# Optimization experiments

Measured on AMD Instinct MI355X. Metric: run time of the kernel, lower is better.

## Reference

```python
import jax, jax.numpy as jnp
import numpy as np

T, H, E = 1024, 2048, 32
I = 1024            # moe_intermediate_size
K = 8               # num_experts_per_token
G = 4               # num_expert_group
TOPK_GROUP = 2
N_SHARED = 2
IS = I * N_SHARED   # shared-expert intermediate
RSF = 2.5           # routed_scaling_factor


def setup_inputs() -> dict:
    key = jax.random.key(0)
    ks = jax.random.split(key, 9)
    s = 0.02
    return {
        "hidden_states": jax.random.normal(ks[0], (T, H), jnp.float32),
        "gate_w": jax.random.normal(ks[1], (H, E), jnp.float32) * s,
        "corr_bias": jax.random.normal(ks[2], (E,), jnp.float32) * s,
        "w_gate": jax.random.normal(ks[3], (E, H, I), jnp.float32) * s,
        "w_up": jax.random.normal(ks[4], (E, H, I), jnp.float32) * s,
        "w_down": jax.random.normal(ks[5], (E, I, H), jnp.float32) * s,
        "sw_gate": jax.random.normal(ks[6], (H, IS), jnp.float32) * s,
        "sw_up": jax.random.normal(ks[7], (H, IS), jnp.float32) * s,
        "sw_down": jax.random.normal(ks[8], (IS, H), jnp.float32) * s,
    }


def _route(x, gate_w, corr_bias):
    # biased grouped top-k (DeepSeek-V3 style sigmoid routing)
    logits = x @ gate_w                      # [T,E]
    scores = jax.nn.sigmoid(logits)
    sfc = scores + corr_bias[None, :]        # scores for choice
    grp = sfc.reshape(-1, G, E // G)
    # group score = sum of top-2 biased scores within the group
    grp_score = jax.lax.top_k(grp, 2)[0].sum(-1)          # [T,G]
    _, gidx = jax.lax.top_k(grp_score, TOPK_GROUP)        # [T,topk_group]
    rows = jnp.arange(sfc.shape[0])[:, None]
    gmask = jnp.zeros((sfc.shape[0], G), sfc.dtype).at[rows, gidx].set(1.0)
    emask = jnp.repeat(gmask, E // G, axis=1)             # [T,E]
    masked = jnp.where(emask > 0, sfc, -jnp.inf)
    _, idx = jax.lax.top_k(masked, K)                     # [T,K]
    w = jnp.take_along_axis(scores, idx, axis=1)          # unbiased scores
    w = w / w.sum(-1, keepdims=True)                      # renormalize
    w = w * RSF                                           # routed scaling
    combine = jnp.zeros((sfc.shape[0], E), x.dtype).at[rows, idx].add(w)
    return combine                                        # dense [T,E] combine weights


def reference(hidden_states, gate_w, corr_bias, w_gate, w_up, w_down,
              sw_gate, sw_up, sw_down):
    x = hidden_states
    # shared experts (SiLU-gated MLP)
    shared = (jax.nn.silu(x @ sw_gate) * (x @ sw_up)) @ sw_down   # [T,H]
    # routing
    combine = _route(x, gate_w, corr_bias)                        # [T,E]
    # routed experts (dense grouped-GEMM reference)
    g = jnp.einsum('th,ehi->tei', x, w_gate)
    u = jnp.einsum('th,ehi->tei', x, w_up)
    a = jax.nn.silu(g) * u                                        # [T,E,I]
    y = jnp.einsum('tei,eih->teh', a, w_down)                     # [T,E,H]
    routed = jnp.einsum('teh,te->th', y, combine)
    return routed + shared
```

## Files before the change

kernel.cpp:

```cpp
#include <hip/hip_runtime.h>

#define T_TOK 1024
#define H_DIM 2048
#define E_NUM 32
#define I_DIM 1024
#define IS_DIM 2048

typedef float  f32x4 __attribute__((ext_vector_type(4)));
typedef short  s16x8 __attribute__((ext_vector_type(8)));
typedef unsigned short u16x4 __attribute__((ext_vector_type(4)));
typedef unsigned short u16x8 __attribute__((ext_vector_type(8)));

__device__ __forceinline__ unsigned short f2bf(float f) {
    unsigned u = __builtin_bit_cast(unsigned, f);
    u = (u + 0x7fffu + ((u >> 16) & 1u)) >> 16;
    return (unsigned short)u;
}
__device__ __forceinline__ float bf2f(unsigned short h) {
    return __builtin_bit_cast(float, (unsigned)h << 16);
}

__device__ __forceinline__ int swzB(int n, int ke) {
    int chunk = (ke >> 3) ^ ((n ^ (n >> 2)) & 15);
    return n * 128 + (chunk << 3) + (ke & 7);
}

__global__ __launch_bounds__(256) void cvt_k(
    const float* __restrict__ x, unsigned short* __restrict__ xb)
{
    const int i = (blockIdx.x * 256 + threadIdx.x) * 8;
    f32x4 a = *(const f32x4*)(x + i);
    f32x4 b = *(const f32x4*)(x + i + 4);
    u16x8 h = { f2bf(a[0]), f2bf(a[1]), f2bf(a[2]), f2bf(a[3]),
                f2bf(b[0]), f2bf(b[1]), f2bf(b[2]), f2bf(b[3]) };
    *(u16x8*)(xb + i) = h;
}

__global__ __launch_bounds__(256) void silu_k(
    const unsigned short* __restrict__ g, const unsigned short* __restrict__ u,
    unsigned short* __restrict__ o)
{
    const int i = (blockIdx.x * 256 + threadIdx.x) * 8;
    u16x8 gv = *(const u16x8*)(g + i);
    u16x8 uv = *(const u16x8*)(u + i);
    u16x8 r;
    #pragma unroll
    for (int j = 0; j < 8; ++j) {
        float gf = bf2f(gv[j]);
        float uf = bf2f(uv[j]);
        r[j] = f2bf(gf / (1.f + expf(-gf)) * uf);
    }
    *(u16x8*)(o + i) = r;
}

__global__ __launch_bounds__(256) void route_k(
    const float* __restrict__ x, const float* __restrict__ gw,
    const float* __restrict__ bias, int* __restrict__ tidx,
    float* __restrict__ tw)
{
    const int w = threadIdx.x >> 6;
    const int lane = threadIdx.x & 63;
    const int t = blockIdx.x * 4 + w;
    __shared__ float xs[4][H_DIM];
    __shared__ float sfc[4][E_NUM];
    __shared__ float sc[4][E_NUM];

    for (int i = threadIdx.x; i < 4 * (H_DIM / 4); i += 256) {
        int tt = i >> 9;
        int c = i & 511;
        *(f32x4*)&xs[tt][c * 4] =
            *(const f32x4*)(x + (size_t)(blockIdx.x * 4 + tt) * H_DIM + c * 4);
    }
    __syncthreads();

    const int eq = (lane & 7) * 4;
    const int hs = lane >> 3;
    f32x4 acc = {0.f, 0.f, 0.f, 0.f};
    #pragma unroll 4
    for (int h = hs; h < H_DIM; h += 8) {
        float xv = xs[w][h];
        f32x4 gv = *(const f32x4*)(gw + (size_t)h * E_NUM + eq);
        acc += gv * xv;
    }
    #pragma unroll
    for (int m = 8; m < 64; m <<= 1) {
        acc[0] += __shfl_xor(acc[0], m);
        acc[1] += __shfl_xor(acc[1], m);
        acc[2] += __shfl_xor(acc[2], m);
        acc[3] += __shfl_xor(acc[3], m);
    }
    if (lane < 8) {
        #pragma unroll
        for (int j = 0; j < 4; ++j) {
            float s = 1.f / (1.f + expf(-acc[j]));
            sc[w][eq + j] = s;
            sfc[w][eq + j] = s + bias[eq + j];
        }
    }
    __syncthreads();

    if (lane == 0) {
        float gs[4];
        for (int gg = 0; gg < 4; ++gg) {
            float m1 = -1e30f, m2 = -1e30f;
            for (int j = 0; j < 8; ++j) {
                float v = sfc[w][gg * 8 + j];
                if (v > m1) { m2 = m1; m1 = v; }
                else if (v > m2) { m2 = v; }
            }
            gs[gg] = m1 + m2;
        }
        int g1 = 0;
        for (int gg = 1; gg < 4; ++gg) if (gs[gg] > gs[g1]) g1 = gg;
        int g2 = (g1 == 0) ? 1 : 0;
        for (int gg = 0; gg < 4; ++gg)
            if (gg != g1 && gs[gg] > gs[g2]) g2 = gg;

        unsigned allow = (0xFFu << (g1 * 8)) | (0xFFu << (g2 * 8));
        unsigned taken = 0u;
        int   isel[8];
        float wsel[8];
        float wsum = 0.f;
        for (int k = 0; k < 8; ++k) {
            int best = 0; float bv = -1e30f;
            for (int e2 = 0; e2 < 32; ++e2) {
                if (((allow >> e2) & 1u) && !((taken >> e2) & 1u)) {
                    float v = sfc[w][e2];
                    if (v > bv) { bv = v; best = e2; }
                }
            }
            taken |= 1u << best;
            isel[k] = best;
            wsel[k] = sc[w][best];
            wsum += sc[w][best];
        }
        const float f = 2.5f / wsum;
        for (int k = 0; k < 8; ++k) {
            tidx[t * 8 + k] = isel[k];
            tw[t * 8 + k] = wsel[k] * f;
        }
    }
}

__global__ __launch_bounds__(64) void build_k(
    const int* __restrict__ tidx, int* __restrict__ ltok,
    int* __restrict__ ppos, int* __restrict__ counts)
{
    const int e = blockIdx.x;
    const int lane = threadIdx.x;
    int cnt = 0;
    for (int t0 = 0; t0 < T_TOK; t0 += 64) {
        const int t = t0 + lane;
        int sel = 0, kk = 0;
        #pragma unroll
        for (int k = 0; k < 8; ++k) {
            if (tidx[t * 8 + k] == e) { sel = 1; kk = k; }
        }
        unsigned long long m = __ballot(sel);
        int pos = __popcll(m & ((1ull << lane) - 1ull));
        if (sel) {
            ltok[e * T_TOK + cnt + pos] = t;
            ppos[t * 8 + kk] = cnt + pos;
        }
        cnt += __popcll(m);
    }
    if (lane == 0) counts[e] = cnt;
}

__global__ void prefix_k(const int* __restrict__ counts, int* __restrict__ offsets)
{
    if (threadIdx.x == 0) {
        int off = 0;
        for (int e = 0; e < E_NUM; ++e) { offsets[e] = off; off += counts[e]; }
    }
}

__global__ __launch_bounds__(256) void combine_k(
    const int* __restrict__ tidx, const float* __restrict__ tw,
    const int* __restrict__ offsets, const int* __restrict__ ppos,
    const unsigned short* __restrict__ shd, const unsigned short* __restrict__ yd,
    float* __restrict__ out)
{
    const int t = blockIdx.x;
    const int h = threadIdx.x * 8;
    u16x8 sv = *(const u16x8*)(shd + (size_t)t * H_DIM + h);
    float a[8];
    #pragma unroll
    for (int j = 0; j < 8; ++j) a[j] = bf2f(sv[j]);
    #pragma unroll
    for (int k = 0; k < 8; ++k) {
        int e = tidx[t * 8 + k];
        float w = tw[t * 8 + k];
        size_t row = (size_t)(offsets[e] + ppos[t * 8 + k]);
        u16x8 v = *(const u16x8*)(yd + row * H_DIM + h);
        #pragma unroll
        for (int j = 0; j < 8; ++j) a[j] += w * bf2f(v[j]);
    }
    f32x4 lo = { a[0], a[1], a[2], a[3] };
    f32x4 hi = { a[4], a[5], a[6], a[7] };
    *(f32x4*)(out + (size_t)t * H_DIM + h)     = lo;
    *(f32x4*)(out + (size_t)t * H_DIM + h + 4) = hi;
}

template<int MSPLIT, int EXPERT, int GATHER, int BM>
__global__ __launch_bounds__(512) void gemm_k(
    const unsigned short* __restrict__ A,
    const float* __restrict__ B1g, const float* __restrict__ B2g,
    unsigned short* __restrict__ out1, unsigned short* __restrict__ out2,
    const int* __restrict__ counts, const int* __restrict__ offsets,
    const int* __restrict__ ltok,
    int M, int N, int K)
{
    constexpr int WR = BM / 4;
    constexpr int FM = WR / 16;

    const int e = blockIdx.z;
    const int Mloc = EXPERT ? counts[e] : M;
    const int rb = EXPERT ? offsets[e] : 0;

    int ymat = 0, ypanel = blockIdx.y;
    if (MSPLIT) {
        const int half = gridDim.y >> 1;
        ymat = (blockIdx.y >= half) ? 1 : 0;
        ypanel -= ymat * half;
    }
    const float* B = ymat ? B2g : B1g;
    unsigned short* outp = ymat ? out2 : out1;
    if (EXPERT) B += (size_t)e * K * N;
    const int colB = ypanel * 64;

    __shared__ unsigned short lB[2][64 * 128];

    const int tid = threadIdx.x;
    const int lane = tid & 63;
    const int wv = tid >> 6;
    const int wm = wv >> 1;
    const int wn = wv & 1;
    const int koff = (lane >> 4) * 8;

    const int nq = tid & 15;
    const int kq = tid >> 4;
    const float* bp = B + (size_t)(4 * kq) * N + colB + nq * 4;

    f32x4 acc[FM][2];
    f32x4 pbX[4], pbY[4];
    const unsigned short* ap[FM];

    auto stageLoad = [&](int k0, f32x4 (&pb)[4]) {
        #pragma unroll
        for (int j = 0; j < 4; ++j)
            pb[j] = *(const f32x4*)(bp + (size_t)(k0 + j) * N);
    };
    auto stageStore = [&](int p, f32x4 (&pb)[4]) {
        #pragma unroll
        for (int j2 = 0; j2 < 4; ++j2) {
            u16x4 h = { f2bf(pb[0][j2]), f2bf(pb[1][j2]),
                        f2bf(pb[2][j2]), f2bf(pb[3][j2]) };
            *(u16x4*)&lB[p][swzB(nq * 4 + j2, kq * 4)] = h;
        }
    };

    const int nk = K >> 7;

    for (int row0 = blockIdx.x * BM; row0 < Mloc; row0 += gridDim.x * BM) {
        #pragma unroll
        for (int fm = 0; fm < FM; ++fm) {
            int rr = row0 + wm * WR + fm * 16 + (lane & 15);
            if (rr >= Mloc) rr = Mloc - 1;
            int grow = GATHER ? ltok[e * T_TOK + rr] : (rb + rr);
            ap[fm] = A + (size_t)grow * K + koff;
        }
        #pragma unroll
        for (int a = 0; a < FM; ++a)
            #pragma unroll
            for (int b = 0; b < 2; ++b)
                acc[a][b] = f32x4{0.f, 0.f, 0.f, 0.f};

        stageLoad(0, pbX);
        stageLoad(128, pbY);
        __syncthreads();
        stageStore(0, pbX);
        __syncthreads();

        for (int kt = 0; kt < nk; ++kt) {
            const int p = kt & 1;
            if (kt + 2 < nk) stageLoad((kt + 2) << 7, p ? pbY : pbX);
            const int kb = kt << 7;
            #pragma unroll
            for (int ks = 0; ks < 4; ++ks) {
                s16x8 af[FM], bf[2];
                #pragma unroll
                for (int fm = 0; fm < FM; ++fm)
                    af[fm] = *(const s16x8*)(ap[fm] + kb + ks * 32);
                #pragma unroll
                for (int fn = 0; fn < 2; ++fn)
                    bf[fn] = *(const s16x8*)&lB[p][swzB(wn * 32 + fn * 16 + (lane & 15),
                                                        ks * 32 + koff)];
                #pragma unroll
                for (int fm = 0; fm < FM; ++fm)
                    #pragma unroll
                    for (int fn = 0; fn < 2; ++fn)
                        acc[fm][fn] = __builtin_amdgcn_mfma_f32_16x16x32_bf16(
                            af[fm], bf[fn], acc[fm][fn], 0, 0, 0);
            }
            if (kt + 1 < nk) {
                stageStore(p ^ 1, p ? pbX : pbY);
                __syncthreads();
            }
        }

        const int fr = (lane >> 4) << 2;
        const int fc = lane & 15;
        #pragma unroll
        for (int fm = 0; fm < FM; ++fm)
            #pragma unroll
            for (int fn = 0; fn < 2; ++fn)
                #pragma unroll
                for (int j = 0; j < 4; ++j) {
                    int r = wm * WR + fm * 16 + fr + j;
                    if (row0 + r < Mloc) {
                        int cc = colB + wn * 32 + fn * 16 + fc;
                        outp[(size_t)(rb + row0 + r) * N + cc] = f2bf(acc[fm][fn][j]);
                    }
                }
    }
}

extern "C" void kernel_launch(void* const* d_in, const int* in_sizes, int n_in,
                              void* d_out, int out_size, void* d_ws, size_t ws_size,
                              hipStream_t stream) {
    const float* x       = (const float*)d_in[0];
    const float* gate_w  = (const float*)d_in[1];
    const float* bias    = (const float*)d_in[2];
    const float* w_gate  = (const float*)d_in[3];
    const float* w_up    = (const float*)d_in[4];
    const float* w_down  = (const float*)d_in[5];
    const float* sw_gate = (const float*)d_in[6];
    const float* sw_up   = (const float*)d_in[7];
    const float* sw_down = (const float*)d_in[8];
    float* out = (float*)d_out;

    char* ws = (char*)d_ws;
    int*   topk_idx = (int*)ws;
    float* topk_w   = (float*)(ws + 32768);
    int*   counts   = (int*)(ws + 65536);
    int*   offsets  = (int*)(ws + 65664);
    int*   ppos     = (int*)(ws + 65792);
    int*   ltok     = (int*)(ws + 98560);
    unsigned short* xbf = (unsigned short*)(ws + 262144);
    unsigned short* g_s = xbf + (size_t)T_TOK * H_DIM;
    unsigned short* u_s = g_s + (size_t)T_TOK * IS_DIM;
    unsigned short* shd = u_s + (size_t)T_TOK * IS_DIM;
    unsigned short* g_r = shd + (size_t)T_TOK * H_DIM;
    unsigned short* u_r = g_r + (size_t)T_TOK * 8 * I_DIM;
    unsigned short* yd  = u_r + (size_t)T_TOK * 8 * I_DIM;

    cvt_k<<<T_TOK * H_DIM / 2048, 256, 0, stream>>>(x, xbf);
    route_k<<<T_TOK / 4, 256, 0, stream>>>(x, gate_w, bias, topk_idx, topk_w);
    build_k<<<E_NUM, 64, 0, stream>>>(topk_idx, ltok, ppos, counts);
    prefix_k<<<1, 64, 0, stream>>>(counts, offsets);

    gemm_k<1,0,0,256><<<dim3(4, 64, 1), 512, 0, stream>>>(
        xbf, sw_gate, sw_up, g_s, u_s, nullptr, nullptr, nullptr,
        T_TOK, IS_DIM, H_DIM);
    silu_k<<<T_TOK * IS_DIM / 2048, 256, 0, stream>>>(g_s, u_s, g_s);

    gemm_k<1,1,1,320><<<dim3(1, 32, E_NUM), 512, 0, stream>>>(
        xbf, w_gate, w_up, g_r, u_r, counts, offsets, ltok,
        T_TOK, I_DIM, H_DIM);
    silu_k<<<T_TOK * 8 * I_DIM / 2048, 256, 0, stream>>>(g_r, u_r, g_r);

    gemm_k<0,0,0,256><<<dim3(4, 32, 1), 512, 0, stream>>>(
        g_s, sw_down, nullptr, shd, nullptr, nullptr, nullptr, nullptr,
        T_TOK, H_DIM, IS_DIM);

    gemm_k<0,1,0,320><<<dim3(1, 32, E_NUM), 512, 0, stream>>>(
        g_r, w_down, nullptr, yd, nullptr, counts, offsets, ltok,
        T_TOK, H_DIM, I_DIM);

    combine_k<<<T_TOK, 256, 0, stream>>>(
        topk_idx, topk_w, offsets, ppos, shd, yd, out);
}
```

Baseline: 850.1 us.

## Stage A tiles through LDS with narrower N panels and 5-wave blocks

The GEMM kernel now stages both A (bf16 activations, gathered per expert) and B (fp32 weights converted to bf16) into double-buffered LDS with a K-step of 32 and an XOR swizzle. Previously A fragments were read straight from global memory. The block changes from 8 waves over a 64-wide N panel to 5 waves of 64 rows each over a 32-wide N panel, with launch bounds of 4 blocks per SM and twice as many N panels launched. The intent is to replace scattered global A reads with coalesced row loads and to raise occupancy. In exchange, each weight column panel is narrower, so A is re-read by twice as many blocks, and there are more barriers per K.

```diff
diff --git a/kernel.cpp b/kernel.cpp
--- a/kernel.cpp
+++ b/kernel.cpp
@@ -8,7 +8,6 @@
 
 typedef float  f32x4 __attribute__((ext_vector_type(4)));
 typedef short  s16x8 __attribute__((ext_vector_type(8)));
-typedef unsigned short u16x4 __attribute__((ext_vector_type(4)));
 typedef unsigned short u16x8 __attribute__((ext_vector_type(8)));
 
 __device__ __forceinline__ unsigned short f2bf(float f) {
@@ -20,9 +19,8 @@
     return __builtin_bit_cast(float, (unsigned)h << 16);
 }
 
-__device__ __forceinline__ int swzB(int n, int ke) {
-    int chunk = (ke >> 3) ^ ((n ^ (n >> 2)) & 15);
-    return n * 128 + (chunk << 3) + (ke & 7);
+__device__ __forceinline__ int swzL(int r, int kchunk) {
+    return r * 32 + ((kchunk ^ (r & 3)) << 3);
 }
 
 __global__ __launch_bounds__(256) void cvt_k(
@@ -202,8 +200,8 @@
     *(f32x4*)(out + (size_t)t * H_DIM + h + 4) = hi;
 }
 
-template<int MSPLIT, int EXPERT, int GATHER, int BM>
-__global__ __launch_bounds__(512) void gemm_k(
+template<int MSPLIT, int EXPERT, int GATHER>
+__global__ __launch_bounds__(320, 4) void gemm_k(
     const unsigned short* __restrict__ A,
     const float* __restrict__ B1g, const float* __restrict__ B2g,
     unsigned short* __restrict__ out1, unsigned short* __restrict__ out2,
@@ -211,8 +209,7 @@
     const int* __restrict__ ltok,
     int M, int N, int K)
 {
-    constexpr int WR = BM / 4;
-    constexpr int FM = WR / 16;
+    constexpr int BM = 320;
 
     const int e = blockIdx.z;
     const int Mloc = EXPERT ? counts[e] : M;
@@ -227,99 +224,111 @@
     const float* B = ymat ? B2g : B1g;
     unsigned short* outp = ymat ? out2 : out1;
     if (EXPERT) B += (size_t)e * K * N;
-    const int colB = ypanel * 64;
-
-    __shared__ unsigned short lB[2][64 * 128];
+    const int colB = ypanel * 32;
+
+    __shared__ unsigned short lA[2][BM * 32];
+    __shared__ unsigned short lB[2][32 * 32];
 
     const int tid = threadIdx.x;
     const int lane = tid & 63;
     const int wv = tid >> 6;
-    const int wm = wv >> 1;
-    const int wn = wv & 1;
-    const int koff = (lane >> 4) * 8;
-
-    const int nq = tid & 15;
-    const int kq = tid >> 4;
-    const float* bp = B + (size_t)(4 * kq) * N + colB + nq * 4;
-
-    f32x4 acc[FM][2];
-    f32x4 pbX[4], pbY[4];
-    const unsigned short* ap[FM];
-
-    auto stageLoad = [&](int k0, f32x4 (&pb)[4]) {
-        #pragma unroll
-        for (int j = 0; j < 4; ++j)
-            pb[j] = *(const f32x4*)(bp + (size_t)(k0 + j) * N);
+    const int q = lane >> 4;
+    const int lr = lane & 15;
+
+    const bool doB = tid < 256;
+    const int nq = tid & 7;
+    const int kr = (tid >> 3) & 31;
+    const float* bp = B + (size_t)kr * N + colB + nq * 4;
+
+    f32x4 acc[4][2];
+    u16x8 paX[4], paY[4];
+    f32x4 pbX, pbY;
+    const unsigned short* apb = nullptr;
+
+    auto loadT = [&](int k0, u16x8 (&pa)[4], f32x4& pb) {
+        #pragma unroll
+        for (int i = 0; i < 4; ++i)
+            pa[i] = *(const u16x8*)(apb + k0 + i * 8);
+        if (doB) pb = *(const f32x4*)(bp + (size_t)k0 * N);
     };
-    auto stageStore = [&](int p, f32x4 (&pb)[4]) {
-        #pragma unroll
-        for (int j2 = 0; j2 < 4; ++j2) {
-            u16x4 h = { f2bf(pb[0][j2]), f2bf(pb[1][j2]),
-                        f2bf(pb[2][j2]), f2bf(pb[3][j2]) };
-            *(u16x4*)&lB[p][swzB(nq * 4 + j2, kq * 4)] = h;
+
+    auto storeT = [&](int p, u16x8 (&pa)[4], f32x4& pb) {
+        #pragma unroll
+        for (int i = 0; i < 4; ++i)
+            *(u16x8*)&lA[p][swzL(tid, i)] = pa[i];
+        if (doB) {
+            #pragma unroll
+            for (int j = 0; j < 4; ++j) {
+                int n = nq * 4 + j;
+                lB[p][n * 32 + (((kr >> 3) ^ (n & 3)) << 3) + (kr & 7)] = f2bf(pb[j]);
+            }
         }
     };
 
-    const int nk = K >> 7;
+    auto compute = [&](int p) {
+        s16x8 af[4], bf[2];
+        #pragma unroll
+        for (int fm = 0; fm < 4; ++fm) {
+            int row = wv * 64 + fm * 16 + lr;
+            af[fm] = *(const s16x8*)&lA[p][swzL(row, q)];
+        }
+        #pragma unroll
+        for (int fn = 0; fn < 2; ++fn) {
+            int n = fn * 16 + lr;
+            bf[fn] = *(const s16x8*)&lB[p][n * 32 + ((q ^ (n & 3)) << 3)];
+        }
+        #pragma unroll
+        for (int fm = 0; fm < 4; ++fm)
+            #pragma unroll
+            for (int fn = 0; fn < 2; ++fn)
+                acc[fm][fn] = __builtin_amdgcn_mfma_f32_16x16x32_bf16(
+                    af[fm], bf[fn], acc[fm][fn], 0, 0, 0);
+    };
+
+    const int nk = K >> 5;
 
     for (int row0 = blockIdx.x * BM; row0 < Mloc; row0 += gridDim.x * BM) {
-        #pragma unroll
-        for (int fm = 0; fm < FM; ++fm) {
-            int rr = row0 + wm * WR + fm * 16 + (lane & 15);
+        {
+            int rr = row0 + tid;
             if (rr >= Mloc) rr = Mloc - 1;
             int grow = GATHER ? ltok[e * T_TOK + rr] : (rb + rr);
-            ap[fm] = A + (size_t)grow * K + koff;
-        }
-        #pragma unroll
-        for (int a = 0; a < FM; ++a)
+            apb = A + (size_t)grow * K;
+        }
+        #pragma unroll
+        for (int a = 0; a < 4; ++a)
             #pragma unroll
             for (int b = 0; b < 2; ++b)
                 acc[a][b] = f32x4{0.f, 0.f, 0.f, 0.f};
 
-        stageLoad(0, pbX);
-        stageLoad(128, pbY);
+        loadT(0, paX, pbX);
+        loadT(32, paY, pbY);
         __syncthreads();
-        stageStore(0, pbX);
+        storeT(0, paX, pbX);
         __syncthreads();
 
-        for (int kt = 0; kt < nk; ++kt) {
-            const int p = kt & 1;
-            if (kt + 2 < nk) stageLoad((kt + 2) << 7, p ? pbY : pbX);
-            const int kb = kt << 7;
-            #pragma unroll
-            for (int ks = 0; ks < 4; ++ks) {
-                s16x8 af[FM], bf[2];
-                #pragma unroll
-                for (int fm = 0; fm < FM; ++fm)
-                    af[fm] = *(const s16x8*)(ap[fm] + kb + ks * 32);
-                #pragma unroll
-                for (int fn = 0; fn < 2; ++fn)
-                    bf[fn] = *(const s16x8*)&lB[p][swzB(wn * 32 + fn * 16 + (lane & 15),
-                                                        ks * 32 + koff)];
-                #pragma unroll
-                for (int fm = 0; fm < FM; ++fm)
-                    #pragma unroll
-                    for (int fn = 0; fn < 2; ++fn)
-                        acc[fm][fn] = __builtin_amdgcn_mfma_f32_16x16x32_bf16(
-                            af[fm], bf[fn], acc[fm][fn], 0, 0, 0);
-            }
-            if (kt + 1 < nk) {
-                stageStore(p ^ 1, p ? pbX : pbY);
+        for (int kt = 0; kt < nk; kt += 2) {
+            if (kt + 2 < nk) loadT((kt + 2) << 5, paX, pbX);
+            compute(0);
+            storeT(1, paY, pbY);
+            __syncthreads();
+            if (kt + 3 < nk) loadT((kt + 3) << 5, paY, pbY);
+            compute(1);
+            if (kt + 2 < nk) {
+                storeT(0, paX, pbX);
                 __syncthreads();
             }
         }
 
-        const int fr = (lane >> 4) << 2;
-        const int fc = lane & 15;
-        #pragma unroll
-        for (int fm = 0; fm < FM; ++fm)
+        const int fr = q << 2;
+        #pragma unroll
+        for (int fm = 0; fm < 4; ++fm)
             #pragma unroll
             for (int fn = 0; fn < 2; ++fn)
                 #pragma unroll
                 for (int j = 0; j < 4; ++j) {
-                    int r = wm * WR + fm * 16 + fr + j;
+                    int r = wv * 64 + fm * 16 + fr + j;
                     if (row0 + r < Mloc) {
-                        int cc = colB + wn * 32 + fn * 16 + fc;
+                        int cc = colB + fn * 16 + lr;
                         outp[(size_t)(rb + row0 + r) * N + cc] = f2bf(acc[fm][fn][j]);
                     }
                 }
@@ -360,21 +369,21 @@
     build_k<<<E_NUM, 64, 0, stream>>>(topk_idx, ltok, ppos, counts);
     prefix_k<<<1, 64, 0, stream>>>(counts, offsets);
 
-    gemm_k<1,0,0,256><<<dim3(4, 64, 1), 512, 0, stream>>>(
+    gemm_k<1,0,0><<<dim3(4, 128, 1), 320, 0, stream>>>(
         xbf, sw_gate, sw_up, g_s, u_s, nullptr, nullptr, nullptr,
         T_TOK, IS_DIM, H_DIM);
     silu_k<<<T_TOK * IS_DIM / 2048, 256, 0, stream>>>(g_s, u_s, g_s);
 
-    gemm_k<1,1,1,320><<<dim3(1, 32, E_NUM), 512, 0, stream>>>(
+    gemm_k<1,1,1><<<dim3(1, 64, E_NUM), 320, 0, stream>>>(
         xbf, w_gate, w_up, g_r, u_r, counts, offsets, ltok,
         T_TOK, I_DIM, H_DIM);
     silu_k<<<T_TOK * 8 * I_DIM / 2048, 256, 0, stream>>>(g_r, u_r, g_r);
 
-    gemm_k<0,0,0,256><<<dim3(4, 32, 1), 512, 0, stream>>>(
+    gemm_k<0,0,0><<<dim3(4, 64, 1), 320, 0, stream>>>(
         g_s, sw_down, nullptr, shd, nullptr, nullptr, nullptr, nullptr,
         T_TOK, H_DIM, IS_DIM);
 
-    gemm_k<0,1,0,320><<<dim3(1, 32, E_NUM), 512, 0, stream>>>(
+    gemm_k<0,1,0><<<dim3(1, 64, E_NUM), 320, 0, stream>>>(
         g_r, w_down, nullptr, yd, nullptr, counts, offsets, ltok,
         T_TOK, H_DIM, I_DIM);
 
```

Result: slower. 1.019 ms (+19.9%).
